# Kernel tuning notes

Measured on AMD Instinct MI355X. Metric: run time of the kernel, lower is better.

Reference implementation:

```python
import jax, jax.numpy as jnp
import numpy as np

DIM = 2048
N_HEADS = 16
N_KV_HEADS = 8
HEAD_DIM = DIM // N_HEADS  # 128
N_REP = N_HEADS // N_KV_HEADS
BATCH = 2
SEQ = 2048
CHUNK = 128  # chunked-parallel causal linear attention; SEQ % CHUNK == 0


def _make_freqs_cis(seq_len, head_dim, theta=10000.0):
    freqs = 1.0 / (theta ** (np.arange(0, head_dim, 2, dtype=np.float32) / head_dim))
    t = np.arange(seq_len, dtype=np.float32)
    ang = np.outer(t, freqs)  # [S, D/2]
    return jnp.asarray(np.stack([np.cos(ang), np.sin(ang)], axis=-1))  # [S, D/2, 2]


def setup_inputs() -> dict:
    key = jax.random.key(0)
    ks = jax.random.split(key, 5)
    x = jax.random.normal(ks[0], (BATCH, SEQ, DIM), dtype=jnp.float32)
    freqs_cis = _make_freqs_cis(SEQ, HEAD_DIM)
    s = 0.02
    wq = s * jax.random.normal(ks[1], (N_HEADS * HEAD_DIM, DIM), dtype=jnp.float32)
    wk = s * jax.random.normal(ks[2], (N_KV_HEADS * HEAD_DIM, DIM), dtype=jnp.float32)
    wv = s * jax.random.normal(ks[3], (N_KV_HEADS * HEAD_DIM, DIM), dtype=jnp.float32)
    wo = s * jax.random.normal(ks[4], (DIM, N_HEADS * HEAD_DIM), dtype=jnp.float32)
    return {"x": x, "freqs_cis": freqs_cis, "wq": wq, "wk": wk, "wv": wv, "wo": wo}


def _apply_rotary(x, freqs_cis):
    # x: [B, S, H, D]; freqs_cis: [S, D/2, 2] (cos, sin). Llama pairing: (x0,x1),(x2,x3),...
    B, S, H, D = x.shape
    xr = x.reshape(B, S, H, D // 2, 2)
    x0, x1 = xr[..., 0], xr[..., 1]
    c = freqs_cis[None, :, None, :, 0]
    s = freqs_cis[None, :, None, :, 1]
    o0 = x0 * c - x1 * s
    o1 = x0 * s + x1 * c
    return jnp.stack([o0, o1], axis=-1).reshape(B, S, H, D)


def _causal_linear_attention(q, k, v):
    # q, k, v: [B, H, S, D]; output_i = q_i @ sum_{j<=i} k_j^T v_j
    B, H, S, D = q.shape
    q = jax.nn.softmax(q * (D ** -0.5), axis=-1)  # softmax over feature dim
    k = jax.nn.softmax(k, axis=2)                 # softmax over sequence dim (as in source)
    Nc = S // CHUNK
    qc = q.reshape(B, H, Nc, CHUNK, D)
    kc = k.reshape(B, H, Nc, CHUNK, D)
    vc = v.reshape(B, H, Nc, CHUNK, D)
    # per-chunk KV outer-product sums: [B, H, Nc, D, D]
    kv = jnp.einsum('bhncd,bhnce->bhnde', kc, vc)
    cum = jnp.cumsum(kv, axis=2)
    cum_excl = jnp.concatenate([jnp.zeros_like(cum[:, :, :1]), cum[:, :, :-1]], axis=2)
    inter = jnp.einsum('bhncd,bhnde->bhnce', qc, cum_excl)
    scores = jnp.einsum('bhncd,bhnmd->bhncm', qc, kc)  # [B,H,Nc,C,C]
    mask = jnp.tril(jnp.ones((CHUNK, CHUNK), dtype=bool))
    scores = jnp.where(mask, scores, jnp.zeros((), dtype=scores.dtype))
    intra = jnp.einsum('bhncm,bhnme->bhnce', scores, vc)
    return (inter + intra).reshape(B, H, S, D)


def reference(x, freqs_cis, wq, wk, wv, wo):
    B, S, _ = x.shape
    xq = (x @ wq.T).reshape(B, S, N_HEADS, HEAD_DIM)
    xk = (x @ wk.T).reshape(B, S, N_KV_HEADS, HEAD_DIM)
    xv = (x @ wv.T).reshape(B, S, N_KV_HEADS, HEAD_DIM)
    xq = _apply_rotary(xq, freqs_cis)
    xk = _apply_rotary(xk, freqs_cis)
    # repeat_kv: each kv head repeated N_REP consecutive times
    keys = jnp.repeat(xk, N_REP, axis=2)
    values = jnp.repeat(xv, N_REP, axis=2)
    q = jnp.transpose(xq, (0, 2, 1, 3))
    k = jnp.transpose(keys, (0, 2, 1, 3))
    v = jnp.transpose(values, (0, 2, 1, 3))
    out = _causal_linear_attention(q, k, v)  # [B, H, S, D]
    out = jnp.transpose(out, (0, 2, 1, 3)).reshape(B, S, N_HEADS * HEAD_DIM)
    return out @ wo.T
```

## Files before the change

### kernel.cpp

```cpp
#include <hip/hip_runtime.h>
#include <math.h>

#define DIMV 2048
#define NHEAD 16
#define NKV 8
#define HD 128
#define BATCH 2
#define SEQ 2048
#define CHUNK 128
#define NCHUNK 16
#define MTOK 4096
#define KVD (NKV * HD)

typedef _Float16 half8_t __attribute__((ext_vector_type(8)));
typedef _Float16 half4_t __attribute__((ext_vector_type(4)));
typedef _Float16 half2_t __attribute__((ext_vector_type(2)));
typedef float f32x4 __attribute__((ext_vector_type(4)));

#define GLOBAL_AS __attribute__((address_space(1)))
#define LDS_AS __attribute__((address_space(3)))

__global__ __launch_bounds__(256) void cast_f2h(const float* __restrict__ in,
                                                _Float16* __restrict__ out, int n) {
  int i = (blockIdx.x * 256 + threadIdx.x) * 8;
  if (i >= n) return;
  float4 a = *(const float4*)&in[i];
  float4 b = *(const float4*)&in[i + 4];
  half8_t h = {(_Float16)a.x, (_Float16)a.y, (_Float16)a.z, (_Float16)a.w,
               (_Float16)b.x, (_Float16)b.y, (_Float16)b.z, (_Float16)b.w};
  *(half8_t*)&out[i] = h;
}

__global__ __launch_bounds__(256) void transpose_fc(const float* __restrict__ fc,
                                                    float* __restrict__ fcT) {
  __shared__ float T[64][65];
  int s0 = blockIdx.x * 64, d0 = blockIdx.y * 64;
  int t = threadIdx.x;
  int r = t >> 4, c4 = (t & 15) * 4;
#pragma unroll
  for (int p = 0; p < 4; ++p) {
    int sr = p * 16 + r;
    float4 v = *(const float4*)&fc[(size_t)(s0 + sr) * 128 + d0 + c4];
    T[sr][c4] = v.x; T[sr][c4 + 1] = v.y; T[sr][c4 + 2] = v.z; T[sr][c4 + 3] = v.w;
  }
  __syncthreads();
#pragma unroll
  for (int p = 0; p < 4; ++p) {
    int dr = p * 16 + r;
    float4 v = make_float4(T[c4][dr], T[c4 + 1][dr], T[c4 + 2][dr], T[c4 + 3][dr]);
    *(float4*)&fcT[(size_t)(d0 + dr) * SEQ + s0 + c4] = v;
  }
}


__global__ __launch_bounds__(256) void hgemm_qkv(const _Float16* __restrict__ A,
                                                 const _Float16* __restrict__ B,
                                                 _Float16* __restrict__ qh,
                                                 _Float16* __restrict__ kT,
                                                 _Float16* __restrict__ vT) {
  const int K = 2048;
  __shared__ _Float16 As[128 * 64];
  __shared__ _Float16 Bs[128 * 64];
  const int tid = threadIdx.x;
  const int lane = tid & 63;
  const int wave = tid >> 6;
  const int row0 = blockIdx.y * 128, col0 = blockIdx.x * 128;
  const int wr = wave & 1, wc = wave >> 1;
  const int m16 = lane & 15, quad = lane >> 4;

  f32x4 acc[4][4];
#pragma unroll
  for (int i = 0; i < 4; ++i)
#pragma unroll
    for (int j = 0; j < 4; ++j) acc[i][j] = (f32x4){0.f, 0.f, 0.f, 0.f};

  const int r_ld = tid >> 3;
  const int sseg = (tid & 7) ^ (r_ld & 7);
  const size_t a_base = (size_t)(row0 + r_ld) * K + sseg * 8;
  const size_t b_base = (size_t)(col0 + r_ld) * K + sseg * 8;
  _Float16* ldsA = As + wave * 512;
  _Float16* ldsB = Bs + wave * 512;
  const int swzA = quad ^ (m16 & 7);

  for (int k0 = 0; k0 < K; k0 += 64) {
#pragma unroll
    for (int i = 0; i < 4; ++i) {
      __builtin_amdgcn_global_load_lds(
          (const GLOBAL_AS void*)(A + a_base + (size_t)i * 32 * K + k0),
          (LDS_AS void*)(ldsA + i * 2048), 16, 0, 0);
      __builtin_amdgcn_global_load_lds(
          (const GLOBAL_AS void*)(B + b_base + (size_t)i * 32 * K + k0),
          (LDS_AS void*)(ldsB + i * 2048), 16, 0, 0);
    }
    __syncthreads();
#pragma unroll
    for (int kk = 0; kk < 2; ++kk) {
      const int swz = swzA ^ (kk * 4);
      half8_t af[4], bf[4];
#pragma unroll
      for (int i = 0; i < 4; ++i) {
        af[i] = *(half8_t*)&As[(wr * 64 + i * 16 + m16) * 64 + swz * 8];
        bf[i] = *(half8_t*)&Bs[(wc * 64 + i * 16 + m16) * 64 + swz * 8];
      }
#pragma unroll
      for (int i = 0; i < 4; ++i)
#pragma unroll
        for (int j = 0; j < 4; ++j)
          acc[i][j] = __builtin_amdgcn_mfma_f32_16x16x32_f16(af[i], bf[j], acc[i][j], 0, 0, 0);
    }
    __syncthreads();
  }

#pragma unroll
  for (int i = 0; i < 4; ++i)
#pragma unroll
    for (int j = 0; j < 4; ++j) {
      int col = col0 + wc * 64 + j * 16 + m16;
      int rowb = row0 + wr * 64 + i * 16 + quad * 4;
      half4_t hv = {(_Float16)acc[i][j][0], (_Float16)acc[i][j][1],
                    (_Float16)acc[i][j][2], (_Float16)acc[i][j][3]};
      if (col0 < 2048) {
#pragma unroll
        for (int r = 0; r < 4; ++r) qh[(size_t)(rowb + r) * DIMV + col] = hv[r];
      } else if (col0 < 3072) {
        *(half4_t*)&kT[(size_t)(col - 2048) * MTOK + rowb] = hv;
      } else {
        *(half4_t*)&vT[(size_t)(col - 3072) * MTOK + rowb] = hv;
      }
    }
}

__global__ __launch_bounds__(256) void hgemm_bt64_f32(const _Float16* __restrict__ A,
                                                      const _Float16* __restrict__ B,
                                                      float* __restrict__ C,
                                                      int M, int N, int K) {
  __shared__ _Float16 As[128 * 64];
  __shared__ _Float16 Bs[128 * 64];
  const int tid = threadIdx.x;
  const int lane = tid & 63;
  const int wave = tid >> 6;
  const int row0 = blockIdx.y * 128, col0 = blockIdx.x * 128;
  const int wr = wave & 1, wc = wave >> 1;
  const int m16 = lane & 15, quad = lane >> 4;

  f32x4 acc[4][4];
#pragma unroll
  for (int i = 0; i < 4; ++i)
#pragma unroll
    for (int j = 0; j < 4; ++j) acc[i][j] = (f32x4){0.f, 0.f, 0.f, 0.f};

  const int r_ld = tid >> 3;
  const int sseg = (tid & 7) ^ (r_ld & 7);
  const size_t a_base = (size_t)(row0 + r_ld) * K + sseg * 8;
  const size_t b_base = (size_t)(col0 + r_ld) * K + sseg * 8;
  _Float16* ldsA = As + wave * 512;
  _Float16* ldsB = Bs + wave * 512;
  const int swzA = quad ^ (m16 & 7);

  for (int k0 = 0; k0 < K; k0 += 64) {
#pragma unroll
    for (int i = 0; i < 4; ++i) {
      __builtin_amdgcn_global_load_lds(
          (const GLOBAL_AS void*)(A + a_base + (size_t)i * 32 * K + k0),
          (LDS_AS void*)(ldsA + i * 2048), 16, 0, 0);
      __builtin_amdgcn_global_load_lds(
          (const GLOBAL_AS void*)(B + b_base + (size_t)i * 32 * K + k0),
          (LDS_AS void*)(ldsB + i * 2048), 16, 0, 0);
    }
    __syncthreads();
#pragma unroll
    for (int kk = 0; kk < 2; ++kk) {
      const int swz = swzA ^ (kk * 4);
      half8_t af[4], bf[4];
#pragma unroll
      for (int i = 0; i < 4; ++i) {
        af[i] = *(half8_t*)&As[(wr * 64 + i * 16 + m16) * 64 + swz * 8];
        bf[i] = *(half8_t*)&Bs[(wc * 64 + i * 16 + m16) * 64 + swz * 8];
      }
#pragma unroll
      for (int i = 0; i < 4; ++i)
#pragma unroll
        for (int j = 0; j < 4; ++j)
          acc[i][j] = __builtin_amdgcn_mfma_f32_16x16x32_f16(af[i], bf[j], acc[i][j], 0, 0, 0);
    }
    __syncthreads();
  }

#pragma unroll
  for (int i = 0; i < 4; ++i)
#pragma unroll
    for (int j = 0; j < 4; ++j) {
      int col = col0 + wc * 64 + j * 16 + m16;
      int rowb = row0 + wr * 64 + i * 16 + quad * 4;
#pragma unroll
      for (int r = 0; r < 4; ++r) C[(size_t)(rowb + r) * N + col] = acc[i][j][r];
    }
}

__global__ __launch_bounds__(64) void rope_q_softmax_h(_Float16* __restrict__ q,
                                                       const float* __restrict__ fc) {
  int bi = blockIdx.x;
  int h = bi & (NHEAD - 1), m = bi >> 4;
  int s = m & (SEQ - 1);
  int t = threadIdx.x;
  size_t base = (size_t)m * DIMV + h * HD + 2 * t;
  half2_t xv = *(const half2_t*)&q[base];
  float2 cs = *(const float2*)&fc[s * HD + 2 * t];
  float x0 = (float)xv[0], x1 = (float)xv[1];
  float o0 = x0 * cs.x - x1 * cs.y;
  float o1 = x0 * cs.y + x1 * cs.x;
  const float sc = 0.08838834764831845f;
  o0 *= sc; o1 *= sc;
  float mx = fmaxf(o0, o1);
#pragma unroll
  for (int off = 1; off < 64; off <<= 1) mx = fmaxf(mx, __shfl_xor(mx, off));
  float e0 = expf(o0 - mx), e1 = expf(o1 - mx);
  float sm = e0 + e1;
#pragma unroll
  for (int off = 1; off < 64; off <<= 1) sm += __shfl_xor(sm, off);
  float inv = 1.f / sm;
  half2_t ov = {(_Float16)(e0 * inv), (_Float16)(e1 * inv)};
  *(half2_t*)&q[base] = ov;
}

__global__ __launch_bounds__(256) void k_rope_softmax_T(_Float16* __restrict__ kT,
                                                        const float* __restrict__ fcT) {
  int bi = blockIdx.x;
  int b = bi & 1, pr = bi >> 1;
  int d0 = pr * 2, dl = d0 & 127;
  int t = threadIdx.x;
  size_t r0 = (size_t)d0 * MTOK + b * SEQ + t * 8;
  size_t r1 = r0 + MTOK;
  half8_t x0v = *(half8_t*)&kT[r0];
  half8_t x1v = *(half8_t*)&kT[r1];
  int s8 = t * 8;
  float4 ca = *(const float4*)&fcT[(size_t)dl * SEQ + s8];
  float4 cb = *(const float4*)&fcT[(size_t)dl * SEQ + s8 + 4];
  float4 sa = *(const float4*)&fcT[(size_t)(dl + 1) * SEQ + s8];
  float4 sb = *(const float4*)&fcT[(size_t)(dl + 1) * SEQ + s8 + 4];
  float cc[8] = {ca.x, ca.y, ca.z, ca.w, cb.x, cb.y, cb.z, cb.w};
  float ss[8] = {sa.x, sa.y, sa.z, sa.w, sb.x, sb.y, sb.z, sb.w};
  float e0[8], e1[8];
  float sum0 = 0.f, sum1 = 0.f;
#pragma unroll
  for (int j = 0; j < 8; ++j) {
    float x0 = (float)x0v[j], x1 = (float)x1v[j];
    float o0 = x0 * cc[j] - x1 * ss[j];
    float o1 = x0 * ss[j] + x1 * cc[j];
    e0[j] = expf(o0); e1[j] = expf(o1);
    sum0 += e0[j]; sum1 += e1[j];
  }
#pragma unroll
  for (int off = 1; off < 64; off <<= 1) {
    sum0 += __shfl_xor(sum0, off);
    sum1 += __shfl_xor(sum1, off);
  }
  __shared__ float red[8];
  if ((t & 63) == 0) { red[(t >> 6) * 2] = sum0; red[(t >> 6) * 2 + 1] = sum1; }
  __syncthreads();
  float S0 = red[0] + red[2] + red[4] + red[6];
  float S1 = red[1] + red[3] + red[5] + red[7];
  float i0 = 1.f / S0, i1 = 1.f / S1;
  half8_t w0, w1;
#pragma unroll
  for (int j = 0; j < 8; ++j) {
    w0[j] = (_Float16)(e0[j] * i0);
    w1[j] = (_Float16)(e1[j] * i1);
  }
  *(half8_t*)&kT[r0] = w0;
  *(half8_t*)&kT[r1] = w1;
}

__global__ __launch_bounds__(256) void transpose_k(const _Float16* __restrict__ kT,
                                                   _Float16* __restrict__ kh) {
  __shared__ _Float16 T[64][65];
  int t0 = blockIdx.x * 64, d0 = blockIdx.y * 64;
  int t = threadIdx.x;
  int r = t >> 3, c8 = (t & 7) * 8;
#pragma unroll
  for (int p = 0; p < 2; ++p) {
    int dr = p * 32 + r;
    half8_t v = *(const half8_t*)&kT[(size_t)(d0 + dr) * MTOK + t0 + c8];
#pragma unroll
    for (int j = 0; j < 8; ++j) T[c8 + j][dr] = v[j];
  }
  __syncthreads();
#pragma unroll
  for (int p = 0; p < 2; ++p) {
    int tr = p * 32 + r;
    half8_t v;
#pragma unroll
    for (int j = 0; j < 8; ++j) v[j] = T[tr][c8 + j];
    *(half8_t*)&kh[(size_t)(t0 + tr) * KVD + d0 + c8] = v;
  }
}

__global__ __launch_bounds__(256) void kv_chunk_mfma(const _Float16* __restrict__ vT,
                                                     const _Float16* __restrict__ kT,
                                                     float* __restrict__ kvT) {
  __shared__ _Float16 As[128 * 32];
  __shared__ _Float16 Bs[128 * 32];
  int bi = blockIdx.x;
  int n = bi & 15, kvh = (bi >> 4) & 7, b = bi >> 7;
  int tok0 = b * SEQ + n * CHUNK;
  const int tid = threadIdx.x;
  const int lane = tid & 63;
  const int wave = tid >> 6;
  const int wr = wave & 1, wc = wave >> 1;
  const int m16 = lane & 15, quad = lane >> 4;

  f32x4 acc[4][4];
#pragma unroll
  for (int i = 0; i < 4; ++i)
#pragma unroll
    for (int j = 0; j < 4; ++j) acc[i][j] = (f32x4){0.f, 0.f, 0.f, 0.f};

  const int r_ld = tid >> 2;
  const int seg = tid & 3;
  const size_t a_base = (size_t)(kvh * HD + r_ld) * MTOK + tok0 + seg * 8;
  const size_t b_base = a_base;
  _Float16* ldsA = As + wave * 512;
  _Float16* ldsB = Bs + wave * 512;

  for (int k0 = 0; k0 < 128; k0 += 32) {
#pragma unroll
    for (int i = 0; i < 2; ++i) {
      __builtin_amdgcn_global_load_lds(
          (const GLOBAL_AS void*)(vT + a_base + (size_t)i * 64 * MTOK + k0),
          (LDS_AS void*)(ldsA + i * 2048), 16, 0, 0);
      __builtin_amdgcn_global_load_lds(
          (const GLOBAL_AS void*)(kT + b_base + (size_t)i * 64 * MTOK + k0),
          (LDS_AS void*)(ldsB + i * 2048), 16, 0, 0);
    }
    __syncthreads();
    half8_t af[4], bf[4];
#pragma unroll
    for (int i = 0; i < 4; ++i) {
      af[i] = *(half8_t*)&As[(wr * 64 + i * 16 + m16) * 32 + quad * 8];
      bf[i] = *(half8_t*)&Bs[(wc * 64 + i * 16 + m16) * 32 + quad * 8];
    }
#pragma unroll
    for (int i = 0; i < 4; ++i)
#pragma unroll
      for (int j = 0; j < 4; ++j)
        acc[i][j] = __builtin_amdgcn_mfma_f32_16x16x32_f16(af[i], bf[j], acc[i][j], 0, 0, 0);
    __syncthreads();
  }
#pragma unroll
  for (int i = 0; i < 4; ++i)
#pragma unroll
    for (int j = 0; j < 4; ++j) {
      int col = wc * 64 + j * 16 + m16;
      int rowb = wr * 64 + i * 16 + quad * 4;
#pragma unroll
      for (int r = 0; r < 4; ++r)
        kvT[(size_t)bi * 16384 + (size_t)(rowb + r) * 128 + col] = acc[i][j][r];
    }
}

__global__ __launch_bounds__(256) void cumsum_h(const float* __restrict__ kvT,
                                                _Float16* __restrict__ cumh) {
  int gid = blockIdx.x * 256 + threadIdx.x;
  int bk = gid >> 14, idx = gid & 16383;
  size_t base = (size_t)bk * NCHUNK * 16384 + idx;
  float run = 0.f;
#pragma unroll
  for (int n = 0; n < NCHUNK; ++n) {
    cumh[base + (size_t)n * 16384] = (_Float16)run;
    run += kvT[base + (size_t)n * 16384];
  }
}

__global__ __launch_bounds__(256) void attn_fused(const _Float16* __restrict__ qh,
                                                  const _Float16* __restrict__ kh,
                                                  const _Float16* __restrict__ cumh,
                                                  const _Float16* __restrict__ vT,
                                                  _Float16* __restrict__ ath) {
  __shared__ _Float16 As[128 * 32];
  __shared__ _Float16 Bs[128 * 32];
  __shared__ _Float16 Ss[128][136];
  int bi = blockIdx.x;
  int n = bi & 15, h = (bi >> 4) & 15, b = bi >> 8;
  int kvh = h >> 1;
  int tok0 = b * SEQ + n * CHUNK;
  const int tid = threadIdx.x;
  const int lane = tid & 63;
  const int wave = tid >> 6;
  const int wr = wave & 1, wc = wave >> 1;
  const int m16 = lane & 15, quad = lane >> 4;
  const int r_ld = tid >> 2;
  const int seg = tid & 3;
  _Float16* ldsA = As + wave * 512;
  _Float16* ldsB = Bs + wave * 512;

  f32x4 acc[4][4];
#pragma unroll
  for (int i = 0; i < 4; ++i)
#pragma unroll
    for (int j = 0; j < 4; ++j) acc[i][j] = (f32x4){0.f, 0.f, 0.f, 0.f};

  const size_t qbase = (size_t)(tok0 + r_ld) * DIMV + h * HD + seg * 8;
  const size_t kbase = (size_t)(tok0 + r_ld) * KVD + kvh * HD + seg * 8;
  const size_t cbase = ((size_t)((b * 8 + kvh) * 16 + n)) * 16384 + (size_t)r_ld * 128 + seg * 8;
  const size_t vbase = (size_t)(kvh * HD + r_ld) * MTOK + tok0 + seg * 8;

  for (int k0 = 0; k0 < 128; k0 += 32) {
#pragma unroll
    for (int i = 0; i < 2; ++i) {
      __builtin_amdgcn_global_load_lds(
          (const GLOBAL_AS void*)(qh + qbase + (size_t)i * 64 * DIMV + k0),
          (LDS_AS void*)(ldsA + i * 2048), 16, 0, 0);
      __builtin_amdgcn_global_load_lds(
          (const GLOBAL_AS void*)(kh + kbase + (size_t)i * 64 * KVD + k0),
          (LDS_AS void*)(ldsB + i * 2048), 16, 0, 0);
    }
    __syncthreads();
    half8_t af[4], bf[4];
#pragma unroll
    for (int i = 0; i < 4; ++i) {
      af[i] = *(half8_t*)&As[(wr * 64 + i * 16 + m16) * 32 + quad * 8];
      bf[i] = *(half8_t*)&Bs[(wc * 64 + i * 16 + m16) * 32 + quad * 8];
    }
#pragma unroll
    for (int i = 0; i < 4; ++i)
#pragma unroll
      for (int j = 0; j < 4; ++j)
        acc[i][j] = __builtin_amdgcn_mfma_f32_16x16x32_f16(af[i], bf[j], acc[i][j], 0, 0, 0);
    __syncthreads();
  }

#pragma unroll
  for (int i = 0; i < 4; ++i)
#pragma unroll
    for (int j = 0; j < 4; ++j) {
      int col = wc * 64 + j * 16 + m16;
      int rowb = wr * 64 + i * 16 + quad * 4;
#pragma unroll
      for (int r = 0; r < 4; ++r) {
        float v = (col <= rowb + r) ? acc[i][j][r] : 0.f;
        Ss[rowb + r][col] = (_Float16)v;
      }
      acc[i][j] = (f32x4){0.f, 0.f, 0.f, 0.f};
    }

  for (int ks = 0; ks < 4; ++ks) {
    int k0 = ks * 32;
#pragma unroll
    for (int i = 0; i < 2; ++i) {
      __builtin_amdgcn_global_load_lds(
          (const GLOBAL_AS void*)(qh + qbase + (size_t)i * 64 * DIMV + k0),
          (LDS_AS void*)(ldsA + i * 2048), 16, 0, 0);
      __builtin_amdgcn_global_load_lds(
          (const GLOBAL_AS void*)(cumh + cbase + (size_t)i * 64 * 128 + k0),
          (LDS_AS void*)(ldsB + i * 2048), 16, 0, 0);
    }
    __syncthreads();
    half8_t af[4], bf[4];
#pragma unroll
    for (int i = 0; i < 4; ++i) {
      af[i] = *(half8_t*)&As[(wr * 64 + i * 16 + m16) * 32 + quad * 8];
      bf[i] = *(half8_t*)&Bs[(wc * 64 + i * 16 + m16) * 32 + quad * 8];
    }
#pragma unroll
    for (int i = 0; i < 4; ++i)
#pragma unroll
      for (int j = 0; j < 4; ++j)
        acc[i][j] = __builtin_amdgcn_mfma_f32_16x16x32_f16(af[i], bf[j], acc[i][j], 0, 0, 0);
    __syncthreads();
  }

  for (int ks = 0; ks < 4; ++ks) {
    int k0 = ks * 32;
#pragma unroll
    for (int i = 0; i < 2; ++i) {
      __builtin_amdgcn_global_load_lds(
          (const GLOBAL_AS void*)(vT + vbase + (size_t)i * 64 * MTOK + k0),
          (LDS_AS void*)(ldsB + i * 2048), 16, 0, 0);
    }
    __syncthreads();
    half8_t af[4], bf[4];
#pragma unroll
    for (int i = 0; i < 4; ++i) {
      af[i] = *(half8_t*)&Ss[wr * 64 + i * 16 + m16][k0 + quad * 8];
      bf[i] = *(half8_t*)&Bs[(wc * 64 + i * 16 + m16) * 32 + quad * 8];
    }
#pragma unroll
    for (int i = 0; i < 4; ++i)
#pragma unroll
      for (int j = 0; j < 4; ++j)
        acc[i][j] = __builtin_amdgcn_mfma_f32_16x16x32_f16(af[i], bf[j], acc[i][j], 0, 0, 0);
    __syncthreads();
  }

#pragma unroll
  for (int i = 0; i < 4; ++i)
#pragma unroll
    for (int j = 0; j < 4; ++j) {
      int col = wc * 64 + j * 16 + m16;
      int rowb = wr * 64 + i * 16 + quad * 4;
#pragma unroll
      for (int r = 0; r < 4; ++r)
        ath[(size_t)(tok0 + rowb + r) * DIMV + h * HD + col] = (_Float16)acc[i][j][r];
    }
}

extern "C" void kernel_launch(void* const* d_in, const int* in_sizes, int n_in,
                              void* d_out, int out_size, void* d_ws, size_t ws_size,
                              hipStream_t stream) {
  const float* x  = (const float*)d_in[0];
  const float* fc = (const float*)d_in[1];
  const float* wq = (const float*)d_in[2];
  const float* wk = (const float*)d_in[3];
  const float* wv = (const float*)d_in[4];
  const float* wo = (const float*)d_in[5];
  float* out = (float*)d_out;

  char* p = (char*)d_ws;
  _Float16* xh    = (_Float16*)p;  p += 16777216;
  _Float16* wqkvh = (_Float16*)p;  p += 16777216;
  _Float16* woh   = (_Float16*)p;  p += 8388608;
  _Float16* qh    = (_Float16*)p;  p += 16777216;
  _Float16* kT    = (_Float16*)p;  p += 8388608;
  _Float16* kh    = (_Float16*)p;  p += 8388608;
  _Float16* vT    = (_Float16*)p;  p += 8388608;
  float*    kvT   = (float*)p;     p += 16777216;
  _Float16* cumh  = (_Float16*)p;  p += 8388608;
  _Float16* ath   = (_Float16*)p;  p += 16777216;
  float*    fcT   = (float*)p;     p += 1048576;

  cast_f2h<<<4096, 256, 0, stream>>>(x, xh, 8388608);
  cast_f2h<<<2048, 256, 0, stream>>>(wq, wqkvh, 4194304);
  cast_f2h<<<1024, 256, 0, stream>>>(wk, wqkvh + 4194304, 2097152);
  cast_f2h<<<1024, 256, 0, stream>>>(wv, wqkvh + 6291456, 2097152);
  cast_f2h<<<2048, 256, 0, stream>>>(wo, woh, 4194304);
  transpose_fc<<<dim3(32, 2), 256, 0, stream>>>(fc, fcT);

  hgemm_qkv<<<dim3(32, 32), 256, 0, stream>>>(xh, wqkvh, qh, kT, vT);

  rope_q_softmax_h<<<MTOK * NHEAD, 64, 0, stream>>>(qh, fc);
  k_rope_softmax_T<<<1024, 256, 0, stream>>>(kT, fcT);
  transpose_k<<<dim3(64, 16), 256, 0, stream>>>(kT, kh);

  kv_chunk_mfma<<<256, 256, 0, stream>>>(vT, kT, kvT);
  cumsum_h<<<1024, 256, 0, stream>>>(kvT, cumh);
  attn_fused<<<512, 256, 0, stream>>>(qh, kh, cumh, vT, ath);

  hgemm_bt64_f32<<<dim3(16, 32), 256, 0, stream>>>(ath, woh, out, MTOK, 2048, 2048);
}
```

Baseline: 315.8 us.

## Fuse Q rotary+softmax into QKV GEMM epilogue and merge cast kernels

Applies rotary embedding and the per-head feature softmax to Q directly in the QKV GEMM epilogue. It uses lane shuffles for the rotary pairs and an LDS reduction across the two column waves for the row sums, and removes the separate rope_q_softmax kernel. It also merges the five fp32-to-fp16 cast launches into a single kernel. The softmax drops max subtraction, which relies on the scaled logits staying small enough not to overflow exp. The epilogue also adds register pressure and a block barrier to the GEMM.

```diff
diff --git a/kernel.cpp b/kernel.cpp
--- a/kernel.cpp
+++ b/kernel.cpp
@@ -20,15 +20,29 @@
 #define GLOBAL_AS __attribute__((address_space(1)))
 #define LDS_AS __attribute__((address_space(3)))
 
-__global__ __launch_bounds__(256) void cast_f2h(const float* __restrict__ in,
-                                                _Float16* __restrict__ out, int n) {
-  int i = (blockIdx.x * 256 + threadIdx.x) * 8;
-  if (i >= n) return;
-  float4 a = *(const float4*)&in[i];
-  float4 b = *(const float4*)&in[i + 4];
+__global__ __launch_bounds__(256) void cast_all(const float* __restrict__ x,
+                                                const float* __restrict__ wq,
+                                                const float* __restrict__ wk,
+                                                const float* __restrict__ wv,
+                                                const float* __restrict__ wo,
+                                                _Float16* __restrict__ xh,
+                                                _Float16* __restrict__ wqkvh,
+                                                _Float16* __restrict__ woh) {
+  long i = (long)(blockIdx.x * 256 + threadIdx.x) * 8;
+  const float* src;
+  _Float16* dst;
+  long off;
+  if (i < 8388608)        { src = x;  dst = xh;              off = 0; }
+  else if (i < 12582912)  { src = wq; dst = wqkvh;           off = 8388608; }
+  else if (i < 14680064)  { src = wk; dst = wqkvh + 4194304; off = 12582912; }
+  else if (i < 16777216)  { src = wv; dst = wqkvh + 6291456; off = 14680064; }
+  else                    { src = wo; dst = woh;             off = 16777216; }
+  long e = i - off;
+  float4 a = *(const float4*)&src[e];
+  float4 b = *(const float4*)&src[e + 4];
   half8_t h = {(_Float16)a.x, (_Float16)a.y, (_Float16)a.z, (_Float16)a.w,
                (_Float16)b.x, (_Float16)b.y, (_Float16)b.z, (_Float16)b.w};
-  *(half8_t*)&out[i] = h;
+  *(half8_t*)&dst[e] = h;
 }
 
 __global__ __launch_bounds__(256) void transpose_fc(const float* __restrict__ fc,
@@ -52,15 +66,16 @@
   }
 }
 
-
 __global__ __launch_bounds__(256) void hgemm_qkv(const _Float16* __restrict__ A,
                                                  const _Float16* __restrict__ B,
+                                                 const float* __restrict__ fc,
                                                  _Float16* __restrict__ qh,
                                                  _Float16* __restrict__ kT,
                                                  _Float16* __restrict__ vT) {
   const int K = 2048;
   __shared__ _Float16 As[128 * 64];
   __shared__ _Float16 Bs[128 * 64];
+  __shared__ float qsum[2][128];
   const int tid = threadIdx.x;
   const int lane = tid & 63;
   const int wave = tid >> 6;
@@ -111,23 +126,78 @@
     __syncthreads();
   }
 
-#pragma unroll
-  for (int i = 0; i < 4; ++i)
-#pragma unroll
-    for (int j = 0; j < 4; ++j) {
-      int col = col0 + wc * 64 + j * 16 + m16;
-      int rowb = row0 + wr * 64 + i * 16 + quad * 4;
-      half4_t hv = {(_Float16)acc[i][j][0], (_Float16)acc[i][j][1],
-                    (_Float16)acc[i][j][2], (_Float16)acc[i][j][3]};
-      if (col0 < 2048) {
-#pragma unroll
-        for (int r = 0; r < 4; ++r) qh[(size_t)(rowb + r) * DIMV + col] = hv[r];
-      } else if (col0 < 3072) {
-        *(half4_t*)&kT[(size_t)(col - 2048) * MTOK + rowb] = hv;
-      } else {
-        *(half4_t*)&vT[(size_t)(col - 3072) * MTOK + rowb] = hv;
-      }
-    }
+  if (col0 < 2048) {
+    const float sc = 0.08838834764831845f;
+    float psum[4][4];
+#pragma unroll
+    for (int i = 0; i < 4; ++i)
+#pragma unroll
+      for (int r = 0; r < 4; ++r) psum[i][r] = 0.f;
+#pragma unroll
+    for (int i = 0; i < 4; ++i)
+#pragma unroll
+      for (int j = 0; j < 4; ++j) {
+        int dl2 = (wc * 64 + j * 16 + m16) & ~1;
+#pragma unroll
+        for (int r = 0; r < 4; ++r) {
+          float val = acc[i][j][r];
+          float par = __shfl_xor(val, 1);
+          int s_tok = (row0 + wr * 64 + i * 16 + quad * 4 + r) & (SEQ - 1);
+          float2 cs = *(const float2*)&fc[(size_t)s_tok * 128 + dl2];
+          float o = val * cs.x + par * ((m16 & 1) ? cs.y : -cs.y);
+          float e = __expf(o * sc);
+          acc[i][j][r] = e;
+          psum[i][r] += e;
+        }
+      }
+#pragma unroll
+    for (int m = 1; m < 16; m <<= 1)
+#pragma unroll
+      for (int i = 0; i < 4; ++i)
+#pragma unroll
+        for (int r = 0; r < 4; ++r) psum[i][r] += __shfl_xor(psum[i][r], m);
+    if (m16 == 0) {
+#pragma unroll
+      for (int i = 0; i < 4; ++i)
+#pragma unroll
+        for (int r = 0; r < 4; ++r)
+          qsum[wc][wr * 64 + i * 16 + quad * 4 + r] = psum[i][r];
+    }
+    __syncthreads();
+#pragma unroll
+    for (int i = 0; i < 4; ++i)
+#pragma unroll
+      for (int r = 0; r < 4; ++r) {
+        int rowl = wr * 64 + i * 16 + quad * 4 + r;
+        psum[i][r] = 1.f / (qsum[0][rowl] + qsum[1][rowl]);
+      }
+#pragma unroll
+    for (int i = 0; i < 4; ++i)
+#pragma unroll
+      for (int j = 0; j < 4; ++j) {
+        int col = col0 + wc * 64 + j * 16 + m16;
+#pragma unroll
+        for (int r = 0; r < 4; ++r) {
+          int row = row0 + wr * 64 + i * 16 + quad * 4 + r;
+          qh[(size_t)row * DIMV + col] = (_Float16)(acc[i][j][r] * psum[i][r]);
+        }
+      }
+  } else {
+#pragma unroll
+    for (int i = 0; i < 4; ++i)
+#pragma unroll
+      for (int j = 0; j < 4; ++j) {
+        int col = col0 + wc * 64 + j * 16 + m16;
+        int rowb = row0 + wr * 64 + i * 16 + quad * 4;
+        half4_t hv = {(_Float16)acc[i][j][0], (_Float16)acc[i][j][1],
+                      (_Float16)acc[i][j][2], (_Float16)acc[i][j][3]};
+        if (col0 < 3072) {
+          *(half4_t*)&kT[(size_t)(col - 2048) * MTOK + rowb] = hv;
+        } else {
+          *(half4_t*)&vT[(size_t)(col - 3072) * MTOK + rowb] = hv;
+        }
+      }
+  }
 }
 
 __global__ __launch_bounds__(256) void hgemm_bt64_f32(const _Float16* __restrict__ A,
@@ -195,32 +265,6 @@
 #pragma unroll
       for (int r = 0; r < 4; ++r) C[(size_t)(rowb + r) * N + col] = acc[i][j][r];
     }
-}
-
-__global__ __launch_bounds__(64) void rope_q_softmax_h(_Float16* __restrict__ q,
-                                                       const float* __restrict__ fc) {
-  int bi = blockIdx.x;
-  int h = bi & (NHEAD - 1), m = bi >> 4;
-  int s = m & (SEQ - 1);
-  int t = threadIdx.x;
-  size_t base = (size_t)m * DIMV + h * HD + 2 * t;
-  half2_t xv = *(const half2_t*)&q[base];
-  float2 cs = *(const float2*)&fc[s * HD + 2 * t];
-  float x0 = (float)xv[0], x1 = (float)xv[1];
-  float o0 = x0 * cs.x - x1 * cs.y;
-  float o1 = x0 * cs.y + x1 * cs.x;
-  const float sc = 0.08838834764831845f;
-  o0 *= sc; o1 *= sc;
-  float mx = fmaxf(o0, o1);
-#pragma unroll
-  for (int off = 1; off < 64; off <<= 1) mx = fmaxf(mx, __shfl_xor(mx, off));
-  float e0 = expf(o0 - mx), e1 = expf(o1 - mx);
-  float sm = e0 + e1;
-#pragma unroll
-  for (int off = 1; off < 64; off <<= 1) sm += __shfl_xor(sm, off);
-  float inv = 1.f / sm;
-  half2_t ov = {(_Float16)(e0 * inv), (_Float16)(e1 * inv)};
-  *(half2_t*)&q[base] = ov;
 }
 
 __global__ __launch_bounds__(256) void k_rope_softmax_T(_Float16* __restrict__ kT,
@@ -528,16 +572,11 @@
   _Float16* ath   = (_Float16*)p;  p += 16777216;
   float*    fcT   = (float*)p;     p += 1048576;
 
-  cast_f2h<<<4096, 256, 0, stream>>>(x, xh, 8388608);
-  cast_f2h<<<2048, 256, 0, stream>>>(wq, wqkvh, 4194304);
-  cast_f2h<<<1024, 256, 0, stream>>>(wk, wqkvh + 4194304, 2097152);
-  cast_f2h<<<1024, 256, 0, stream>>>(wv, wqkvh + 6291456, 2097152);
-  cast_f2h<<<2048, 256, 0, stream>>>(wo, woh, 4194304);
+  cast_all<<<10240, 256, 0, stream>>>(x, wq, wk, wv, wo, xh, wqkvh, woh);
   transpose_fc<<<dim3(32, 2), 256, 0, stream>>>(fc, fcT);
 
-  hgemm_qkv<<<dim3(32, 32), 256, 0, stream>>>(xh, wqkvh, qh, kT, vT);
-
-  rope_q_softmax_h<<<MTOK * NHEAD, 64, 0, stream>>>(qh, fc);
+  hgemm_qkv<<<dim3(32, 32), 256, 0, stream>>>(xh, wqkvh, fc, qh, kT, vT);
+
   k_rope_softmax_T<<<1024, 256, 0, stream>>>(kT, fcT);
   transpose_k<<<dim3(64, 16), 256, 0, stream>>>(kT, kh);
 
```

After: 300.8 us. 4.8% less time.
